# Optimization experiments

Hardware: AMD Instinct MI355X
Metric: run time of the kernel (lower is better)

Reference implementation:

```python
import jax, jax.numpy as jnp
import numpy as np

ROUNDS = 2
N_NODES = 50000
N_EDGES = 800000
NODE_DIM = 128
EDGE_DIM = 32
ACT_DIM = 128


def setup_inputs() -> dict:
    key = jax.random.key(0)
    ks = jax.random.split(key, 10)
    hv = jax.random.normal(ks[0], (N_NODES, NODE_DIM), dtype=jnp.float32)
    he = jax.random.normal(ks[1], (N_EDGES, EDGE_DIM), dtype=jnp.float32)
    src = jax.random.randint(ks[2], (N_EDGES,), 0, N_NODES, dtype=jnp.int32)
    dst = jax.random.randint(ks[3], (N_EDGES,), 0, N_NODES, dtype=jnp.int32)
    cat_dim = 2 * NODE_DIM + EDGE_DIM  # 288
    W_msg = jax.random.normal(ks[4], (ROUNDS, cat_dim, ACT_DIM), dtype=jnp.float32) * 0.05
    b_msg = jax.random.normal(ks[5], (ROUNDS, ACT_DIM), dtype=jnp.float32) * 0.05
    W_ih = jax.random.normal(ks[6], (ROUNDS, ACT_DIM, 3 * NODE_DIM), dtype=jnp.float32) * 0.05
    W_hh = jax.random.normal(ks[7], (ROUNDS, NODE_DIM, 3 * NODE_DIM), dtype=jnp.float32) * 0.05
    b_ih = jax.random.normal(ks[8], (ROUNDS, 3 * NODE_DIM), dtype=jnp.float32) * 0.05
    b_hh = jax.random.normal(ks[9], (ROUNDS, 3 * NODE_DIM), dtype=jnp.float32) * 0.05
    return {"hv": hv, "he": he, "src": src, "dst": dst,
            "W_msg": W_msg, "b_msg": b_msg,
            "W_ih": W_ih, "W_hh": W_hh, "b_ih": b_ih, "b_hh": b_hh}


def _gru_cell(x, h, W_ih, W_hh, b_ih, b_hh):
    # torch.nn.GRUCell math, gate order (r, z, n)
    gi = x @ W_ih + b_ih  # [N, 3H]
    gh = h @ W_hh + b_hh  # [N, 3H]
    ir, iz, in_ = jnp.split(gi, 3, axis=-1)
    hr, hz, hn = jnp.split(gh, 3, axis=-1)
    r = jax.nn.sigmoid(ir + hr)
    z = jax.nn.sigmoid(iz + hz)
    n = jnp.tanh(in_ + r * hn)
    return (1.0 - z) * n + z * h


def reference(hv, he, src, dst, W_msg, b_msg, W_ih, W_hh, b_ih, b_hh):
    N, nd = hv.shape
    for t in range(ROUNDS):
        # Linear on concat([hv_src, hv_dst, he]) == sum of block matmuls
        Ws = W_msg[t, :nd]          # src block
        Wd = W_msg[t, nd:2 * nd]    # dst block
        We = W_msg[t, 2 * nd:]      # edge block
        msg = hv[src] @ Ws + hv[dst] @ Wd + he @ We + b_msg[t]  # [E, act]
        a = jax.ops.segment_sum(msg, dst, num_segments=N)        # per-node sum over incoming edges
        hv = _gru_cell(a, hv, W_ih[t], W_hh[t], b_ih[t], b_hh[t])
    return hv
```

## Files before the change

kernel.cpp:

```cpp
#include <hip/hip_runtime.h>

#define N_NODES 50000
#define N_EDGES 800000
#define ND 128
#define ED 32
#define AD 128
#define CAT 288
#define G3 384

#define XP2 168
#define SCAN_BS 512

typedef unsigned short ushort_t;
typedef __attribute__((ext_vector_type(8))) short bfrag;
typedef __attribute__((ext_vector_type(4))) float f32x4;

__device__ __forceinline__ unsigned int f2bf(float f) {
    unsigned int u = __float_as_uint(f);
    return (u + 0x7FFFu + ((u >> 16) & 1u)) >> 16;
}
__device__ __forceinline__ void split2(float a, float b,
                                       unsigned int& hi, unsigned int& lo) {
    const unsigned int ha = f2bf(a), hb = f2bf(b);
    const float ra = a - __uint_as_float(ha << 16);
    const float rb = b - __uint_as_float(hb << 16);
    hi = ha | (hb << 16);
    lo = f2bf(ra) | (f2bf(rb) << 16);
}
__device__ __forceinline__ void split1(float a, ushort_t& hi, ushort_t& lo) {
    const unsigned int ha = f2bf(a);
    const float ra = a - __uint_as_float(ha << 16);
    hi = (ushort_t)ha;
    lo = (ushort_t)f2bf(ra);
}

__global__ __launch_bounds__(256) void hist_kernel(
    const int* __restrict__ dst, int* __restrict__ deg)
{
    const int e = blockIdx.x * 256 + threadIdx.x;
    if (e < N_EDGES) atomicAdd(&deg[dst[e]], 1);
}

__global__ __launch_bounds__(SCAN_BS) void scan_block_kernel(
    const int* __restrict__ in, int* __restrict__ out,
    int* __restrict__ bsum, int n)
{
    __shared__ int s[SCAN_BS];
    const int g = blockIdx.x * SCAN_BS + threadIdx.x;
    const int v = (g < n) ? in[g] : 0;
    s[threadIdx.x] = v;
    __syncthreads();
    for (int off = 1; off < SCAN_BS; off <<= 1) {
        const int x = (threadIdx.x >= off) ? s[threadIdx.x - off] : 0;
        __syncthreads();
        s[threadIdx.x] += x;
        __syncthreads();
    }
    if (g < n) out[g] = s[threadIdx.x] - v;
    if (threadIdx.x == SCAN_BS - 1) bsum[blockIdx.x] = s[threadIdx.x];
}

__global__ __launch_bounds__(128) void scan_sums_kernel(int* __restrict__ bsum, int nb)
{
    __shared__ int s[128];
    const int i = threadIdx.x;
    s[i] = (i < nb) ? bsum[i] : 0;
    __syncthreads();
    if (i == 0) {
        int acc = 0;
        for (int k = 0; k < nb; ++k) { const int t = s[k]; s[k] = acc; acc += t; }
    }
    __syncthreads();
    if (i < nb) bsum[i] = s[i];
}

__global__ __launch_bounds__(SCAN_BS) void scan_add_kernel(
    int* __restrict__ rowptr, int* __restrict__ cursor,
    const int* __restrict__ bsum, int n)
{
    const int g = blockIdx.x * SCAN_BS + threadIdx.x;
    if (g < n) {
        const int v = rowptr[g] + bsum[blockIdx.x];
        rowptr[g] = v;
        cursor[g] = v;
    }
}

__global__ __launch_bounds__(256) void fill_kernel(
    const int* __restrict__ dst, const int* __restrict__ src,
    int* __restrict__ cursor, int* __restrict__ perm,
    int* __restrict__ src_sorted)
{
    const int e = blockIdx.x * 256 + threadIdx.x;
    if (e < N_EDGES) {
        const int p = atomicAdd(&cursor[dst[e]], 1);
        perm[p] = e;
        src_sorted[p] = src[e];
    }
}

__global__ __launch_bounds__(256) void esum_kernel(
    const float* __restrict__ he, const int* __restrict__ perm,
    const int* __restrict__ rowptr, float* __restrict__ E)
{
    const int id = blockIdx.x * 256 + threadIdx.x;
    if (id >= N_NODES * ED) return;
    const int v = id >> 5, c = id & 31;
    const int r0 = rowptr[v], r1 = rowptr[v + 1];
    float s = 0.f;
    int i = r0;
    for (; i + 4 <= r1; i += 4) {
        const int p0 = perm[i],     p1 = perm[i + 1];
        const int p2 = perm[i + 2], p3 = perm[i + 3];
        const float a = he[(size_t)p0 * ED + c];
        const float b = he[(size_t)p1 * ED + c];
        const float d = he[(size_t)p2 * ED + c];
        const float f = he[(size_t)p3 * ED + c];
        s += (a + b) + (d + f);
    }
    for (; i < r1; ++i)
        s += he[(size_t)perm[i] * ED + c];
    E[(size_t)v * ED + c] = s;
}

__global__ __launch_bounds__(256) void convert_w_kernel(
    const float* __restrict__ W,
    ushort_t* __restrict__ Wt_hi, ushort_t* __restrict__ Wt_lo)
{
    const int id = blockIdx.x * 256 + threadIdx.x;
    if (id >= 2 * CAT * AD) return;
    const int tt = id / (CAT * AD);
    const int q  = id % (CAT * AD);
    const int j  = q & 7;
    const int lr = (q >> 3) & 15;
    const int kq = (q >> 7) & 3;
    const int ks = (q >> 9) % 9;
    const int gnt = q / 4608;
    const int n  = gnt * 16 + lr;
    const int kn = ks * 32 + kq * 8 + j;
    const int ko = kn < 128 ? kn : (kn < 160 ? kn + 128 : kn - 32);
    const float w = W[(size_t)tt * CAT * AD + (size_t)ko * AD + n];
    const unsigned int hi = f2bf(w);
    const float r = w - __uint_as_float(hi << 16);
    const size_t o = (size_t)tt * (CAT * AD) + q;
    Wt_hi[o] = (ushort_t)hi;
    Wt_lo[o] = (ushort_t)f2bf(r);
}

__global__ __launch_bounds__(256) void convert_gatew_kernel(
    const float* __restrict__ W_ih, const float* __restrict__ W_hh,
    ushort_t* __restrict__ Bih_hi, ushort_t* __restrict__ Bih_lo,
    ushort_t* __restrict__ Bhh_hi, ushort_t* __restrict__ Bhh_lo)
{
    const int id = blockIdx.x * 256 + threadIdx.x;
    if (id >= 196608) return;
    const int t   = id / 98304;
    const int rem = id % 98304;
    const int mat = rem / 49152;
    const int q   = rem % 49152;
    const int nt = q / 2048,  r1 = q % 2048;
    const int ks = r1 / 512,  r2 = r1 % 512;
    const int kq = r2 / 128,  r3 = r2 % 128;
    const int lr = r3 / 8,    j  = r3 % 8;
    const int wv = nt / 6, within = nt % 6;
    const int gate = within % 3, hf = within / 3;
    const int n = gate * 128 + wv * 32 + hf * 16 + lr;
    const int k = ks * 32 + kq * 8 + j;
    const float* W = mat ? W_hh : W_ih;
    const float w = W[(size_t)t * ND * G3 + (size_t)k * G3 + n];
    const unsigned int hi = f2bf(w);
    const float res = w - __uint_as_float(hi << 16);
    const size_t o = (size_t)t * 49152 + q;
    if (mat) { Bhh_hi[o] = (ushort_t)hi; Bhh_lo[o] = (ushort_t)f2bf(res); }
    else     { Bih_hi[o] = (ushort_t)hi; Bih_lo[o] = (ushort_t)f2bf(res); }
}

__global__ __launch_bounds__(256) void agg_kernel(
    const float* __restrict__ hv, const int* __restrict__ src_sorted,
    const int* __restrict__ rowptr,
    ushort_t* __restrict__ S_hi, ushort_t* __restrict__ S_lo)
{
    const int v = blockIdx.x * 4 + (threadIdx.x >> 6);
    if (v >= N_NODES) return;
    const int lane = threadIdx.x & 63;
    const int r0 = rowptr[v], r1 = rowptr[v + 1];
    const float2* hv2 = (const float2*)hv;
    float sx = 0.f, sy = 0.f;
    int i = r0;
    for (; i + 8 <= r1; i += 8) {
        const int s0 = src_sorted[i],     s1 = src_sorted[i + 1];
        const int s2 = src_sorted[i + 2], s3 = src_sorted[i + 3];
        const int s4 = src_sorted[i + 4], s5 = src_sorted[i + 5];
        const int s6 = src_sorted[i + 6], s7 = src_sorted[i + 7];
        const float2 a = hv2[(size_t)s0 * 64 + lane];
        const float2 b = hv2[(size_t)s1 * 64 + lane];
        const float2 c = hv2[(size_t)s2 * 64 + lane];
        const float2 d = hv2[(size_t)s3 * 64 + lane];
        const float2 e = hv2[(size_t)s4 * 64 + lane];
        const float2 f = hv2[(size_t)s5 * 64 + lane];
        const float2 g = hv2[(size_t)s6 * 64 + lane];
        const float2 h = hv2[(size_t)s7 * 64 + lane];
        sx += ((a.x + b.x) + (c.x + d.x)) + ((e.x + f.x) + (g.x + h.x));
        sy += ((a.y + b.y) + (c.y + d.y)) + ((e.y + f.y) + (g.y + h.y));
    }
    for (; i < r1; ++i) {
        const float2 a = hv2[(size_t)src_sorted[i] * 64 + lane];
        sx += a.x; sy += a.y;
    }
    unsigned int h, l;
    split2(sx, sy, h, l);
    ((unsigned int*)S_hi)[(size_t)v * 64 + lane] = h;
    ((unsigned int*)S_lo)[(size_t)v * 64 + lane] = l;
}

__global__ __launch_bounds__(256, 3) void fused_msg_gru_kernel(
    const ushort_t* __restrict__ S_hi, const ushort_t* __restrict__ S_lo,
    const float* __restrict__ h_cur, const float* __restrict__ E,
    const int* __restrict__ rowptr,
    const ushort_t* __restrict__ Wt_hi, const ushort_t* __restrict__ Wt_lo,
    const float* __restrict__ bmsg,
    const ushort_t* __restrict__ Bih_hi, const ushort_t* __restrict__ Bih_lo,
    const ushort_t* __restrict__ Bhh_hi, const ushort_t* __restrict__ Bhh_lo,
    const float* __restrict__ b_ih, const float* __restrict__ b_hh,
    float* __restrict__ h_out)
{
    __shared__ __align__(16) char smem[37888];
    ushort_t* xh    = (ushort_t*)smem;
    ushort_t* xl    = xh + 32 * XP2;
    ushort_t* sh_hi = xl + 32 * XP2;
    ushort_t* sh_lo = sh_hi + 32 * 128;
    ushort_t* sa_hi = (ushort_t*)smem;
    ushort_t* sa_lo = sa_hi + 32 * 128;
    __shared__ float sdeg[32];

    const int t    = threadIdx.x;
    const int wave = t >> 6;
    const int lane = t & 63;
    const int kq   = lane >> 4;
    const int lr   = lane & 15;
    const int n0   = blockIdx.x * 32;

    const float mbias0 = bmsg[wave * 32 + lr];
    const float mbias1 = bmsg[wave * 32 + 16 + lr];

    {
        const int row = t >> 3, c8 = t & 7;
        const int n = min(n0 + row, N_NODES - 1);
        if (t < 32) {
            const int nn = min(n0 + t, N_NODES - 1);
            sdeg[t] = (float)(rowptr[nn + 1] - rowptr[nn]);
        }
        {
            const uint4* ph = (const uint4*)(S_hi + (size_t)n * ND + c8 * 16);
            const uint4* pl = (const uint4*)(S_lo + (size_t)n * ND + c8 * 16);
            *(uint4*)&xh[row * XP2 + c8 * 16]     = ph[0];
            *(uint4*)&xh[row * XP2 + c8 * 16 + 8] = ph[1];
            *(uint4*)&xl[row * XP2 + c8 * 16]     = pl[0];
            *(uint4*)&xl[row * XP2 + c8 * 16 + 8] = pl[1];
        }
        {
            const float4* hp = (const float4*)(h_cur + (size_t)n * ND + c8 * 16);
            const float4 v0 = hp[0], v1 = hp[1], v2 = hp[2], v3 = hp[3];
            uint4 h0, h1, l0, l1;
            split2(v0.x, v0.y, h0.x, l0.x); split2(v0.z, v0.w, h0.y, l0.y);
            split2(v1.x, v1.y, h0.z, l0.z); split2(v1.z, v1.w, h0.w, l0.w);
            split2(v2.x, v2.y, h1.x, l1.x); split2(v2.z, v2.w, h1.y, l1.y);
            split2(v3.x, v3.y, h1.z, l1.z); split2(v3.z, v3.w, h1.w, l1.w);
            const int so  = (row * 128 + c8 * 16)     ^ ((row & 7) << 3);
            const int so2 = (row * 128 + c8 * 16 + 8) ^ ((row & 7) << 3);
            *(uint4*)(sh_hi + so)  = h0;  *(uint4*)(sh_hi + so2) = h1;
            *(uint4*)(sh_lo + so)  = l0;  *(uint4*)(sh_lo + so2) = l1;
        }
        {
            const float4 e4 = *(const float4*)(E + (size_t)n * ED + c8 * 4);
            uint2 h0, l0;
            split2(e4.x, e4.y, h0.x, l0.x); split2(e4.z, e4.w, h0.y, l0.y);
            *(uint2*)&xh[row * XP2 + 128 + c8 * 4] = h0;
            *(uint2*)&xl[row * XP2 + 128 + c8 * 4] = l0;
        }
    }
    __syncthreads();

    f32x4 aX00 = {0.f,0.f,0.f,0.f}, aX01 = {0.f,0.f,0.f,0.f};
    f32x4 aX10 = {0.f,0.f,0.f,0.f}, aX11 = {0.f,0.f,0.f,0.f};
    f32x4 aP00 = {0.f,0.f,0.f,0.f}, aP01 = {0.f,0.f,0.f,0.f};
    f32x4 aP10 = {0.f,0.f,0.f,0.f}, aP11 = {0.f,0.f,0.f,0.f};
    {
        const size_t wb0 = (size_t)(wave * 2 + 0) * 4608 + kq * 128 + lr * 8;
        const size_t wb1 = (size_t)(wave * 2 + 1) * 4608 + kq * 128 + lr * 8;
        const ushort_t* wh0 = Wt_hi + wb0;  const ushort_t* wl0 = Wt_lo + wb0;
        const ushort_t* wh1 = Wt_hi + wb1;  const ushort_t* wl1 = Wt_lo + wb1;
        #pragma unroll
        for (int ks = 0; ks < 5; ++ks) {
            const int ko = ks * 32 + kq * 8;
            const bfrag a0h = *(const bfrag*)&xh[lr * XP2 + ko];
            const bfrag a0l = *(const bfrag*)&xl[lr * XP2 + ko];
            const bfrag a1h = *(const bfrag*)&xh[(16 + lr) * XP2 + ko];
            const bfrag a1l = *(const bfrag*)&xl[(16 + lr) * XP2 + ko];
            const bfrag b0h = *(const bfrag*)(wh0 + ks * 512);
            const bfrag b0l = *(const bfrag*)(wl0 + ks * 512);
            const bfrag b1h = *(const bfrag*)(wh1 + ks * 512);
            const bfrag b1l = *(const bfrag*)(wl1 + ks * 512);
            aX00 = __builtin_amdgcn_mfma_f32_16x16x32_bf16(a0h, b0h, aX00, 0, 0, 0);
            aX00 = __builtin_amdgcn_mfma_f32_16x16x32_bf16(a0l, b0h, aX00, 0, 0, 0);
            aX00 = __builtin_amdgcn_mfma_f32_16x16x32_bf16(a0h, b0l, aX00, 0, 0, 0);
            aX01 = __builtin_amdgcn_mfma_f32_16x16x32_bf16(a0h, b1h, aX01, 0, 0, 0);
            aX01 = __builtin_amdgcn_mfma_f32_16x16x32_bf16(a0l, b1h, aX01, 0, 0, 0);
            aX01 = __builtin_amdgcn_mfma_f32_16x16x32_bf16(a0h, b1l, aX01, 0, 0, 0);
            aX10 = __builtin_amdgcn_mfma_f32_16x16x32_bf16(a1h, b0h, aX10, 0, 0, 0);
            aX10 = __builtin_amdgcn_mfma_f32_16x16x32_bf16(a1l, b0h, aX10, 0, 0, 0);
            aX10 = __builtin_amdgcn_mfma_f32_16x16x32_bf16(a1h, b0l, aX10, 0, 0, 0);
            aX11 = __builtin_amdgcn_mfma_f32_16x16x32_bf16(a1h, b1h, aX11, 0, 0, 0);
            aX11 = __builtin_amdgcn_mfma_f32_16x16x32_bf16(a1l, b1h, aX11, 0, 0, 0);
            aX11 = __builtin_amdgcn_mfma_f32_16x16x32_bf16(a1h, b1l, aX11, 0, 0, 0);
        }
        #pragma unroll
        for (int ks = 5; ks < 9; ++ks) {
            const int hk = (ks - 5) * 32 + kq * 8;
            const int o0 = (lr * 128 + hk)        ^ ((lr & 7) << 3);
            const int o1 = ((16 + lr) * 128 + hk) ^ ((lr & 7) << 3);
            const bfrag a0h = *(const bfrag*)(sh_hi + o0);
            const bfrag a0l = *(const bfrag*)(sh_lo + o0);
            const bfrag a1h = *(const bfrag*)(sh_hi + o1);
            const bfrag a1l = *(const bfrag*)(sh_lo + o1);
            const bfrag b0h = *(const bfrag*)(wh0 + ks * 512);
            const bfrag b0l = *(const bfrag*)(wl0 + ks * 512);
            const bfrag b1h = *(const bfrag*)(wh1 + ks * 512);
            const bfrag b1l = *(const bfrag*)(wl1 + ks * 512);
            aP00 = __builtin_amdgcn_mfma_f32_16x16x32_bf16(a0h, b0h, aP00, 0, 0, 0);
            aP00 = __builtin_amdgcn_mfma_f32_16x16x32_bf16(a0l, b0h, aP00, 0, 0, 0);
            aP00 = __builtin_amdgcn_mfma_f32_16x16x32_bf16(a0h, b0l, aP00, 0, 0, 0);
            aP01 = __builtin_amdgcn_mfma_f32_16x16x32_bf16(a0h, b1h, aP01, 0, 0, 0);
            aP01 = __builtin_amdgcn_mfma_f32_16x16x32_bf16(a0l, b1h, aP01, 0, 0, 0);
            aP01 = __builtin_amdgcn_mfma_f32_16x16x32_bf16(a0h, b1l, aP01, 0, 0, 0);
            aP10 = __builtin_amdgcn_mfma_f32_16x16x32_bf16(a1h, b0h, aP10, 0, 0, 0);
            aP10 = __builtin_amdgcn_mfma_f32_16x16x32_bf16(a1l, b0h, aP10, 0, 0, 0);
            aP10 = __builtin_amdgcn_mfma_f32_16x16x32_bf16(a1h, b0l, aP10, 0, 0, 0);
            aP11 = __builtin_amdgcn_mfma_f32_16x16x32_bf16(a1h, b1h, aP11, 0, 0, 0);
            aP11 = __builtin_amdgcn_mfma_f32_16x16x32_bf16(a1l, b1h, aP11, 0, 0, 0);
            aP11 = __builtin_amdgcn_mfma_f32_16x16x32_bf16(a1h, b1l, aP11, 0, 0, 0);
        }
    }
    __syncthreads();

    #pragma unroll
    for (int r = 0; r < 4; ++r) {
        const int row0 = kq * 4 + r;
        const int row1 = 16 + row0;
        const int c0 = wave * 32 + lr, c1 = c0 + 16;
        const float d0 = sdeg[row0], d1 = sdeg[row1];
        ushort_t h, l;
        split1(aX00[r] + d0 * (aP00[r] + mbias0), h, l);
        { const int o = (row0 * 128 + c0) ^ ((row0 & 7) << 3); sa_hi[o] = h; sa_lo[o] = l; }
        split1(aX01[r] + d0 * (aP01[r] + mbias1), h, l);
        { const int o = (row0 * 128 + c1) ^ ((row0 & 7) << 3); sa_hi[o] = h; sa_lo[o] = l; }
        split1(aX10[r] + d1 * (aP10[r] + mbias0), h, l);
        { const int o = (row1 * 128 + c0) ^ ((row1 & 7) << 3); sa_hi[o] = h; sa_lo[o] = l; }
        split1(aX11[r] + d1 * (aP11[r] + mbias1), h, l);
        { const int o = (row1 * 128 + c1) ^ ((row1 & 7) << 3); sa_hi[o] = h; sa_lo[o] = l; }
    }
    __syncthreads();

    #pragma unroll
    for (int half = 0; half < 2; ++half) {
        f32x4 ai[2][3], ah2[2][3];
        #pragma unroll
        for (int m = 0; m < 2; ++m)
            #pragma unroll
            for (int g = 0; g < 3; ++g) {
                ai[m][g]  = (f32x4){0.f, 0.f, 0.f, 0.f};
                ah2[m][g] = (f32x4){0.f, 0.f, 0.f, 0.f};
            }
        #pragma unroll
        for (int ks = 0; ks < 4; ++ks) {
            bfrag afh[2], afl[2], hfh[2], hfl[2];
            #pragma unroll
            for (int m = 0; m < 2; ++m) {
                const int o = ((m * 16 + lr) * 128 + ks * 32 + kq * 8) ^ ((lr & 7) << 3);
                afh[m] = *(const bfrag*)(sa_hi + o);
                afl[m] = *(const bfrag*)(sa_lo + o);
                hfh[m] = *(const bfrag*)(sh_hi + o);
                hfl[m] = *(const bfrag*)(sh_lo + o);
            }
            #pragma unroll
            for (int g = 0; g < 3; ++g) {
                const int gnt = wave * 6 + half * 3 + g;
                const size_t bo = (size_t)(gnt * 2048 + ks * 512 + kq * 128 + lr * 8);
                const bfrag bih_h = *(const bfrag*)(Bih_hi + bo);
                const bfrag bih_l = *(const bfrag*)(Bih_lo + bo);
                const bfrag bhh_h = *(const bfrag*)(Bhh_hi + bo);
                const bfrag bhh_l = *(const bfrag*)(Bhh_lo + bo);
                #pragma unroll
                for (int m = 0; m < 2; ++m) {
                    ai[m][g]  = __builtin_amdgcn_mfma_f32_16x16x32_bf16(afh[m], bih_h, ai[m][g], 0, 0, 0);
                    ai[m][g]  = __builtin_amdgcn_mfma_f32_16x16x32_bf16(afl[m], bih_h, ai[m][g], 0, 0, 0);
                    ai[m][g]  = __builtin_amdgcn_mfma_f32_16x16x32_bf16(afh[m], bih_l, ai[m][g], 0, 0, 0);
                    ah2[m][g] = __builtin_amdgcn_mfma_f32_16x16x32_bf16(hfh[m], bhh_h, ah2[m][g], 0, 0, 0);
                    ah2[m][g] = __builtin_amdgcn_mfma_f32_16x16x32_bf16(hfl[m], bhh_h, ah2[m][g], 0, 0, 0);
                    ah2[m][g] = __builtin_amdgcn_mfma_f32_16x16x32_bf16(hfh[m], bhh_l, ah2[m][g], 0, 0, 0);
                }
            }
        }
        const int c = wave * 32 + half * 16 + lr;
        const float br  = b_ih[c] + b_hh[c];
        const float bz  = b_ih[128 + c] + b_hh[128 + c];
        const float bin = b_ih[256 + c];
        const float bhn = b_hh[256 + c];
        #pragma unroll
        for (int m = 0; m < 2; ++m)
            #pragma unroll
            for (int r = 0; r < 4; ++r) {
                const int nn = n0 + m * 16 + kq * 4 + r;
                if (nn < N_NODES) {
                    const float hc = h_cur[(size_t)nn * ND + c];
                    const float rg = 1.f / (1.f + __expf(-(ai[m][0][r] + ah2[m][0][r] + br)));
                    const float zg = 1.f / (1.f + __expf(-(ai[m][1][r] + ah2[m][1][r] + bz)));
                    const float npre = ai[m][2][r] + bin + rg * (ah2[m][2][r] + bhn);
                    const float ng = 1.f - 2.f / (__expf(2.f * npre) + 1.f);
                    h_out[(size_t)nn * ND + c] = (1.f - zg) * ng + zg * hc;
                }
            }
    }
}

extern "C" void kernel_launch(void* const* d_in, const int* in_sizes, int n_in,
                              void* d_out, int out_size, void* d_ws, size_t ws_size,
                              hipStream_t stream)
{
    const float* hv   = (const float*)d_in[0];
    const float* he   = (const float*)d_in[1];
    const int*   src  = (const int*)d_in[2];
    const int*   dst  = (const int*)d_in[3];
    const float* Wmsg = (const float*)d_in[4];
    const float* bmsg = (const float*)d_in[5];
    const float* Wih  = (const float*)d_in[6];
    const float* Whh  = (const float*)d_in[7];
    const float* bih  = (const float*)d_in[8];
    const float* bhh  = (const float*)d_in[9];
    float* out = (float*)d_out;

    const int nscan = ((N_NODES + SCAN_BS - 1) / SCAN_BS) * SCAN_BS;
    const int nblk  = nscan / SCAN_BS;

    char* p = (char*)d_ws;
    ushort_t* S_hi = (ushort_t*)p;            p += (size_t)N_NODES * ND * 2;
    ushort_t* S_lo = (ushort_t*)p;            p += (size_t)N_NODES * ND * 2;
    float* E = (float*)p;                     p += (size_t)N_NODES * ED * 4;
    ushort_t* Wt_hi = (ushort_t*)p;           p += (size_t)2 * AD * CAT * 2;
    ushort_t* Wt_lo = (ushort_t*)p;           p += (size_t)2 * AD * CAT * 2;
    ushort_t* Bih_hi = (ushort_t*)p;          p += (size_t)2 * G3 * ND * 2;
    ushort_t* Bih_lo = (ushort_t*)p;          p += (size_t)2 * G3 * ND * 2;
    ushort_t* Bhh_hi = (ushort_t*)p;          p += (size_t)2 * G3 * ND * 2;
    ushort_t* Bhh_lo = (ushort_t*)p;          p += (size_t)2 * G3 * ND * 2;
    int* deg    = (int*)p;                    p += (size_t)nscan * 4;
    int* rowptr = (int*)p;                    p += (size_t)nscan * 4;
    int* cursor = (int*)p;                    p += (size_t)nscan * 4;
    int* bsum   = (int*)p;                    p += 128 * 4;
    int* perm   = (int*)p;                    p += (size_t)N_EDGES * 4;
    int* src_sorted = (int*)p;                p += (size_t)N_EDGES * 4;

    convert_w_kernel<<<(2 * CAT * AD + 255) / 256, 256, 0, stream>>>(Wmsg, Wt_hi, Wt_lo);
    convert_gatew_kernel<<<768, 256, 0, stream>>>(Wih, Whh, Bih_hi, Bih_lo, Bhh_hi, Bhh_lo);

    hipMemsetAsync(deg, 0, (size_t)nscan * 4, stream);
    hist_kernel<<<(N_EDGES + 255) / 256, 256, 0, stream>>>(dst, deg);
    scan_block_kernel<<<nblk, SCAN_BS, 0, stream>>>(deg, rowptr, bsum, nscan);
    scan_sums_kernel<<<1, 128, 0, stream>>>(bsum, nblk);
    scan_add_kernel<<<nblk, SCAN_BS, 0, stream>>>(rowptr, cursor, bsum, nscan);
    fill_kernel<<<(N_EDGES + 255) / 256, 256, 0, stream>>>(dst, src, cursor, perm, src_sorted);
    esum_kernel<<<(N_NODES * ED + 255) / 256, 256, 0, stream>>>(he, perm, rowptr, E);

    const int tile_blocks = (N_NODES + 31) / 32;

    for (int t = 0; t < 2; ++t) {
        const float* h_cur = (t == 0) ? hv : out;
        agg_kernel<<<(N_NODES + 3) / 4, 256, 0, stream>>>(
            h_cur, src_sorted, rowptr, S_hi, S_lo);
        fused_msg_gru_kernel<<<tile_blocks, 256, 0, stream>>>(
            S_hi, S_lo, h_cur, E, rowptr,
            Wt_hi + (size_t)t * AD * CAT, Wt_lo + (size_t)t * AD * CAT,
            bmsg + (size_t)t * AD,
            Bih_hi + (size_t)t * G3 * ND, Bih_lo + (size_t)t * G3 * ND,
            Bhh_hi + (size_t)t * G3 * ND, Bhh_lo + (size_t)t * G3 * ND,
            bih + (size_t)t * G3, bhh + (size_t)t * G3, out);
    }
}
```

Baseline: 528.8 us.

## Enlarge fused GRU tile to 64 nodes and stage output through shared memory

Doubles the node tile per block from 32 to 64 rows, so each weight fragment loaded from global memory feeds four MFMA row tiles instead of two. The r/z gate input and hidden products are folded into one accumulator, which cuts register use. Outputs are staged in shared memory and written back as coalesced float4 rows. The cost is twice the LDS per block, launch bounds lowered from 3 to 2 blocks per CU, and extra syncs, so latency hiding may drop.

```diff
diff --git a/kernel.cpp b/kernel.cpp
--- a/kernel.cpp
+++ b/kernel.cpp
@@ -8,6 +8,7 @@
 #define CAT 288
 #define G3 384
 
+#define MT 64
 #define XP2 168
 #define SCAN_BS 512
 
@@ -213,7 +214,7 @@
     ((unsigned int*)S_lo)[(size_t)v * 64 + lane] = l;
 }
 
-__global__ __launch_bounds__(256, 3) void fused_msg_gru_kernel(
+__global__ __launch_bounds__(256, 2) void fused_msg_gru_kernel(
     const ushort_t* __restrict__ S_hi, const ushort_t* __restrict__ S_lo,
     const float* __restrict__ h_cur, const float* __restrict__ E,
     const int* __restrict__ rowptr,
@@ -224,67 +225,75 @@
     const float* __restrict__ b_ih, const float* __restrict__ b_hh,
     float* __restrict__ h_out)
 {
-    __shared__ __align__(16) char smem[37888];
+    __shared__ __align__(16) char smem[75776];
     ushort_t* xh    = (ushort_t*)smem;
-    ushort_t* xl    = xh + 32 * XP2;
-    ushort_t* sh_hi = xl + 32 * XP2;
-    ushort_t* sh_lo = sh_hi + 32 * 128;
+    ushort_t* xl    = xh + MT * XP2;
+    ushort_t* sh_hi = xl + MT * XP2;
+    ushort_t* sh_lo = sh_hi + MT * 128;
     ushort_t* sa_hi = (ushort_t*)smem;
-    ushort_t* sa_lo = sa_hi + 32 * 128;
-    __shared__ float sdeg[32];
+    ushort_t* sa_lo = sa_hi + MT * 128;
+    float* out_s = (float*)smem;
+    __shared__ float sdeg[MT];
 
     const int t    = threadIdx.x;
     const int wave = t >> 6;
     const int lane = t & 63;
     const int kq   = lane >> 4;
     const int lr   = lane & 15;
-    const int n0   = blockIdx.x * 32;
+    const int n0   = blockIdx.x * MT;
 
     const float mbias0 = bmsg[wave * 32 + lr];
     const float mbias1 = bmsg[wave * 32 + 16 + lr];
 
     {
-        const int row = t >> 3, c8 = t & 7;
+        const int row = t >> 2, q = t & 3;
         const int n = min(n0 + row, N_NODES - 1);
-        if (t < 32) {
+        if (t < MT) {
             const int nn = min(n0 + t, N_NODES - 1);
             sdeg[t] = (float)(rowptr[nn + 1] - rowptr[nn]);
         }
         {
-            const uint4* ph = (const uint4*)(S_hi + (size_t)n * ND + c8 * 16);
-            const uint4* pl = (const uint4*)(S_lo + (size_t)n * ND + c8 * 16);
-            *(uint4*)&xh[row * XP2 + c8 * 16]     = ph[0];
-            *(uint4*)&xh[row * XP2 + c8 * 16 + 8] = ph[1];
-            *(uint4*)&xl[row * XP2 + c8 * 16]     = pl[0];
-            *(uint4*)&xl[row * XP2 + c8 * 16 + 8] = pl[1];
+            const uint4* ph = (const uint4*)(S_hi + (size_t)n * ND + q * 32);
+            const uint4* pl = (const uint4*)(S_lo + (size_t)n * ND + q * 32);
+            #pragma unroll
+            for (int j = 0; j < 4; ++j) {
+                *(uint4*)&xh[row * XP2 + q * 32 + j * 8] = ph[j];
+                *(uint4*)&xl[row * XP2 + q * 32 + j * 8] = pl[j];
+            }
         }
         {
-            const float4* hp = (const float4*)(h_cur + (size_t)n * ND + c8 * 16);
-            const float4 v0 = hp[0], v1 = hp[1], v2 = hp[2], v3 = hp[3];
-            uint4 h0, h1, l0, l1;
-            split2(v0.x, v0.y, h0.x, l0.x); split2(v0.z, v0.w, h0.y, l0.y);
-            split2(v1.x, v1.y, h0.z, l0.z); split2(v1.z, v1.w, h0.w, l0.w);
-            split2(v2.x, v2.y, h1.x, l1.x); split2(v2.z, v2.w, h1.y, l1.y);
-            split2(v3.x, v3.y, h1.z, l1.z); split2(v3.z, v3.w, h1.w, l1.w);
-            const int so  = (row * 128 + c8 * 16)     ^ ((row & 7) << 3);
-            const int so2 = (row * 128 + c8 * 16 + 8) ^ ((row & 7) << 3);
-            *(uint4*)(sh_hi + so)  = h0;  *(uint4*)(sh_hi + so2) = h1;
-            *(uint4*)(sh_lo + so)  = l0;  *(uint4*)(sh_lo + so2) = l1;
+            const float4* hp = (const float4*)(h_cur + (size_t)n * ND + q * 32);
+            #pragma unroll
+            for (int j = 0; j < 4; ++j) {
+                const float4 va = hp[2 * j], vb = hp[2 * j + 1];
+                uint4 hh, ll;
+                split2(va.x, va.y, hh.x, ll.x); split2(va.z, va.w, hh.y, ll.y);
+                split2(vb.x, vb.y, hh.z, ll.z); split2(vb.z, vb.w, hh.w, ll.w);
+                const int so = (row * 128 + q * 32 + j * 8) ^ ((row & 7) << 3);
+                *(uint4*)(sh_hi + so) = hh;
+                *(uint4*)(sh_lo + so) = ll;
+            }
         }
         {
-            const float4 e4 = *(const float4*)(E + (size_t)n * ED + c8 * 4);
-            uint2 h0, l0;
-            split2(e4.x, e4.y, h0.x, l0.x); split2(e4.z, e4.w, h0.y, l0.y);
-            *(uint2*)&xh[row * XP2 + 128 + c8 * 4] = h0;
-            *(uint2*)&xl[row * XP2 + 128 + c8 * 4] = l0;
-        }
-    }
-    __syncthreads();
-
-    f32x4 aX00 = {0.f,0.f,0.f,0.f}, aX01 = {0.f,0.f,0.f,0.f};
-    f32x4 aX10 = {0.f,0.f,0.f,0.f}, aX11 = {0.f,0.f,0.f,0.f};
-    f32x4 aP00 = {0.f,0.f,0.f,0.f}, aP01 = {0.f,0.f,0.f,0.f};
-    f32x4 aP10 = {0.f,0.f,0.f,0.f}, aP11 = {0.f,0.f,0.f,0.f};
+            const float4 e0 = *(const float4*)(E + (size_t)n * ED + q * 8);
+            const float4 e1 = *(const float4*)(E + (size_t)n * ED + q * 8 + 4);
+            uint4 eh, el;
+            split2(e0.x, e0.y, eh.x, el.x); split2(e0.z, e0.w, eh.y, el.y);
+            split2(e1.x, e1.y, eh.z, el.z); split2(e1.z, e1.w, eh.w, el.w);
+            *(uint4*)&xh[row * XP2 + 128 + q * 8] = eh;
+            *(uint4*)&xl[row * XP2 + 128 + q * 8] = el;
+        }
+    }
+    __syncthreads();
+
+    f32x4 aX[4][2], aP[4][2];
+    #pragma unroll
+    for (int m = 0; m < 4; ++m)
+        #pragma unroll
+        for (int nt = 0; nt < 2; ++nt) {
+            aX[m][nt] = (f32x4){0.f, 0.f, 0.f, 0.f};
+            aP[m][nt] = (f32x4){0.f, 0.f, 0.f, 0.f};
+        }
     {
         const size_t wb0 = (size_t)(wave * 2 + 0) * 4608 + kq * 128 + lr * 8;
         const size_t wb1 = (size_t)(wave * 2 + 1) * 4608 + kq * 128 + lr * 8;
@@ -293,89 +302,76 @@
         #pragma unroll
         for (int ks = 0; ks < 5; ++ks) {
             const int ko = ks * 32 + kq * 8;
-            const bfrag a0h = *(const bfrag*)&xh[lr * XP2 + ko];
-            const bfrag a0l = *(const bfrag*)&xl[lr * XP2 + ko];
-            const bfrag a1h = *(const bfrag*)&xh[(16 + lr) * XP2 + ko];
-            const bfrag a1l = *(const bfrag*)&xl[(16 + lr) * XP2 + ko];
             const bfrag b0h = *(const bfrag*)(wh0 + ks * 512);
             const bfrag b0l = *(const bfrag*)(wl0 + ks * 512);
             const bfrag b1h = *(const bfrag*)(wh1 + ks * 512);
             const bfrag b1l = *(const bfrag*)(wl1 + ks * 512);
-            aX00 = __builtin_amdgcn_mfma_f32_16x16x32_bf16(a0h, b0h, aX00, 0, 0, 0);
-            aX00 = __builtin_amdgcn_mfma_f32_16x16x32_bf16(a0l, b0h, aX00, 0, 0, 0);
-            aX00 = __builtin_amdgcn_mfma_f32_16x16x32_bf16(a0h, b0l, aX00, 0, 0, 0);
-            aX01 = __builtin_amdgcn_mfma_f32_16x16x32_bf16(a0h, b1h, aX01, 0, 0, 0);
-            aX01 = __builtin_amdgcn_mfma_f32_16x16x32_bf16(a0l, b1h, aX01, 0, 0, 0);
-            aX01 = __builtin_amdgcn_mfma_f32_16x16x32_bf16(a0h, b1l, aX01, 0, 0, 0);
-            aX10 = __builtin_amdgcn_mfma_f32_16x16x32_bf16(a1h, b0h, aX10, 0, 0, 0);
-            aX10 = __builtin_amdgcn_mfma_f32_16x16x32_bf16(a1l, b0h, aX10, 0, 0, 0);
-            aX10 = __builtin_amdgcn_mfma_f32_16x16x32_bf16(a1h, b0l, aX10, 0, 0, 0);
-            aX11 = __builtin_amdgcn_mfma_f32_16x16x32_bf16(a1h, b1h, aX11, 0, 0, 0);
-            aX11 = __builtin_amdgcn_mfma_f32_16x16x32_bf16(a1l, b1h, aX11, 0, 0, 0);
-            aX11 = __builtin_amdgcn_mfma_f32_16x16x32_bf16(a1h, b1l, aX11, 0, 0, 0);
+            #pragma unroll
+            for (int m = 0; m < 4; ++m) {
+                const bfrag ah_ = *(const bfrag*)&xh[(m * 16 + lr) * XP2 + ko];
+                const bfrag al_ = *(const bfrag*)&xl[(m * 16 + lr) * XP2 + ko];
+                aX[m][0] = __builtin_amdgcn_mfma_f32_16x16x32_bf16(ah_, b0h, aX[m][0], 0, 0, 0);
+                aX[m][0] = __builtin_amdgcn_mfma_f32_16x16x32_bf16(al_, b0h, aX[m][0], 0, 0, 0);
+                aX[m][0] = __builtin_amdgcn_mfma_f32_16x16x32_bf16(ah_, b0l, aX[m][0], 0, 0, 0);
+                aX[m][1] = __builtin_amdgcn_mfma_f32_16x16x32_bf16(ah_, b1h, aX[m][1], 0, 0, 0);
+                aX[m][1] = __builtin_amdgcn_mfma_f32_16x16x32_bf16(al_, b1h, aX[m][1], 0, 0, 0);
+                aX[m][1] = __builtin_amdgcn_mfma_f32_16x16x32_bf16(ah_, b1l, aX[m][1], 0, 0, 0);
+            }
         }
         #pragma unroll
         for (int ks = 5; ks < 9; ++ks) {
             const int hk = (ks - 5) * 32 + kq * 8;
-            const int o0 = (lr * 128 + hk)        ^ ((lr & 7) << 3);
-            const int o1 = ((16 + lr) * 128 + hk) ^ ((lr & 7) << 3);
-            const bfrag a0h = *(const bfrag*)(sh_hi + o0);
-            const bfrag a0l = *(const bfrag*)(sh_lo + o0);
-            const bfrag a1h = *(const bfrag*)(sh_hi + o1);
-            const bfrag a1l = *(const bfrag*)(sh_lo + o1);
             const bfrag b0h = *(const bfrag*)(wh0 + ks * 512);
             const bfrag b0l = *(const bfrag*)(wl0 + ks * 512);
             const bfrag b1h = *(const bfrag*)(wh1 + ks * 512);
             const bfrag b1l = *(const bfrag*)(wl1 + ks * 512);
-            aP00 = __builtin_amdgcn_mfma_f32_16x16x32_bf16(a0h, b0h, aP00, 0, 0, 0);
-            aP00 = __builtin_amdgcn_mfma_f32_16x16x32_bf16(a0l, b0h, aP00, 0, 0, 0);
-            aP00 = __builtin_amdgcn_mfma_f32_16x16x32_bf16(a0h, b0l, aP00, 0, 0, 0);
-            aP01 = __builtin_amdgcn_mfma_f32_16x16x32_bf16(a0h, b1h, aP01, 0, 0, 0);
-            aP01 = __builtin_amdgcn_mfma_f32_16x16x32_bf16(a0l, b1h, aP01, 0, 0, 0);
-            aP01 = __builtin_amdgcn_mfma_f32_16x16x32_bf16(a0h, b1l, aP01, 0, 0, 0);
-            aP10 = __builtin_amdgcn_mfma_f32_16x16x32_bf16(a1h, b0h, aP10, 0, 0, 0);
-            aP10 = __builtin_amdgcn_mfma_f32_16x16x32_bf16(a1l, b0h, aP10, 0, 0, 0);
-            aP10 = __builtin_amdgcn_mfma_f32_16x16x32_bf16(a1h, b0l, aP10, 0, 0, 0);
-            aP11 = __builtin_amdgcn_mfma_f32_16x16x32_bf16(a1h, b1h, aP11, 0, 0, 0);
-            aP11 = __builtin_amdgcn_mfma_f32_16x16x32_bf16(a1l, b1h, aP11, 0, 0, 0);
-            aP11 = __builtin_amdgcn_mfma_f32_16x16x32_bf16(a1h, b1l, aP11, 0, 0, 0);
+            #pragma unroll
+            for (int m = 0; m < 4; ++m) {
+                const int o = ((m * 16 + lr) * 128 + hk) ^ ((lr & 7) << 3);
+                const bfrag ah_ = *(const bfrag*)(sh_hi + o);
+                const bfrag al_ = *(const bfrag*)(sh_lo + o);
+                aP[m][0] = __builtin_amdgcn_mfma_f32_16x16x32_bf16(ah_, b0h, aP[m][0], 0, 0, 0);
+                aP[m][0] = __builtin_amdgcn_mfma_f32_16x16x32_bf16(al_, b0h, aP[m][0], 0, 0, 0);
+                aP[m][0] = __builtin_amdgcn_mfma_f32_16x16x32_bf16(ah_, b0l, aP[m][0], 0, 0, 0);
+                aP[m][1] = __builtin_amdgcn_mfma_f32_16x16x32_bf16(ah_, b1h, aP[m][1], 0, 0, 0);
+                aP[m][1] = __builtin_amdgcn_mfma_f32_16x16x32_bf16(al_, b1h, aP[m][1], 0, 0, 0);
+                aP[m][1] = __builtin_amdgcn_mfma_f32_16x16x32_bf16(ah_, b1l, aP[m][1], 0, 0, 0);
+            }
         }
     }
     __syncthreads();
 
     #pragma unroll
-    for (int r = 0; r < 4; ++r) {
-        const int row0 = kq * 4 + r;
-        const int row1 = 16 + row0;
-        const int c0 = wave * 32 + lr, c1 = c0 + 16;
-        const float d0 = sdeg[row0], d1 = sdeg[row1];
-        ushort_t h, l;
-        split1(aX00[r] + d0 * (aP00[r] + mbias0), h, l);
-        { const int o = (row0 * 128 + c0) ^ ((row0 & 7) << 3); sa_hi[o] = h; sa_lo[o] = l; }
-        split1(aX01[r] + d0 * (aP01[r] + mbias1), h, l);
-        { const int o = (row0 * 128 + c1) ^ ((row0 & 7) << 3); sa_hi[o] = h; sa_lo[o] = l; }
-        split1(aX10[r] + d1 * (aP10[r] + mbias0), h, l);
-        { const int o = (row1 * 128 + c0) ^ ((row1 & 7) << 3); sa_hi[o] = h; sa_lo[o] = l; }
-        split1(aX11[r] + d1 * (aP11[r] + mbias1), h, l);
-        { const int o = (row1 * 128 + c1) ^ ((row1 & 7) << 3); sa_hi[o] = h; sa_lo[o] = l; }
-    }
-    __syncthreads();
-
+    for (int m = 0; m < 4; ++m)
+        #pragma unroll
+        for (int r = 0; r < 4; ++r) {
+            const int row = m * 16 + kq * 4 + r;
+            const int c0 = wave * 32 + lr, c1 = c0 + 16;
+            const float d = sdeg[row];
+            ushort_t h, l;
+            split1(aX[m][0][r] + d * (aP[m][0][r] + mbias0), h, l);
+            { const int o = (row * 128 + c0) ^ ((row & 7) << 3); sa_hi[o] = h; sa_lo[o] = l; }
+            split1(aX[m][1][r] + d * (aP[m][1][r] + mbias1), h, l);
+            { const int o = (row * 128 + c1) ^ ((row & 7) << 3); sa_hi[o] = h; sa_lo[o] = l; }
+        }
+    __syncthreads();
+
+    float outv[2][4][4];
     #pragma unroll
     for (int half = 0; half < 2; ++half) {
-        f32x4 ai[2][3], ah2[2][3];
-        #pragma unroll
-        for (int m = 0; m < 2; ++m)
-            #pragma unroll
-            for (int g = 0; g < 3; ++g) {
-                ai[m][g]  = (f32x4){0.f, 0.f, 0.f, 0.f};
-                ah2[m][g] = (f32x4){0.f, 0.f, 0.f, 0.f};
-            }
+        f32x4 arz[4][2], anI[4], anH[4];
+        #pragma unroll
+        for (int m = 0; m < 4; ++m) {
+            arz[m][0] = (f32x4){0.f, 0.f, 0.f, 0.f};
+            arz[m][1] = (f32x4){0.f, 0.f, 0.f, 0.f};
+            anI[m]    = (f32x4){0.f, 0.f, 0.f, 0.f};
+            anH[m]    = (f32x4){0.f, 0.f, 0.f, 0.f};
+        }
         #pragma unroll
         for (int ks = 0; ks < 4; ++ks) {
-            bfrag afh[2], afl[2], hfh[2], hfl[2];
-            #pragma unroll
-            for (int m = 0; m < 2; ++m) {
+            bfrag afh[4], afl[4], hfh[4], hfl[4];
+            #pragma unroll
+            for (int m = 0; m < 4; ++m) {
                 const int o = ((m * 16 + lr) * 128 + ks * 32 + kq * 8) ^ ((lr & 7) << 3);
                 afh[m] = *(const bfrag*)(sa_hi + o);
                 afl[m] = *(const bfrag*)(sa_lo + o);
@@ -390,14 +386,28 @@
                 const bfrag bih_l = *(const bfrag*)(Bih_lo + bo);
                 const bfrag bhh_h = *(const bfrag*)(Bhh_hi + bo);
                 const bfrag bhh_l = *(const bfrag*)(Bhh_lo + bo);
-                #pragma unroll
-                for (int m = 0; m < 2; ++m) {
-                    ai[m][g]  = __builtin_amdgcn_mfma_f32_16x16x32_bf16(afh[m], bih_h, ai[m][g], 0, 0, 0);
-                    ai[m][g]  = __builtin_amdgcn_mfma_f32_16x16x32_bf16(afl[m], bih_h, ai[m][g], 0, 0, 0);
-                    ai[m][g]  = __builtin_amdgcn_mfma_f32_16x16x32_bf16(afh[m], bih_l, ai[m][g], 0, 0, 0);
-                    ah2[m][g] = __builtin_amdgcn_mfma_f32_16x16x32_bf16(hfh[m], bhh_h, ah2[m][g], 0, 0, 0);
-                    ah2[m][g] = __builtin_amdgcn_mfma_f32_16x16x32_bf16(hfl[m], bhh_h, ah2[m][g], 0, 0, 0);
-                    ah2[m][g] = __builtin_amdgcn_mfma_f32_16x16x32_bf16(hfh[m], bhh_l, ah2[m][g], 0, 0, 0);
+                if (g < 2) {
+                    #pragma unroll
+                    for (int m = 0; m < 4; ++m) {
+                        f32x4 a = arz[m][g];
+                        a = __builtin_amdgcn_mfma_f32_16x16x32_bf16(afh[m], bih_h, a, 0, 0, 0);
+                        a = __builtin_amdgcn_mfma_f32_16x16x32_bf16(afl[m], bih_h, a, 0, 0, 0);
+                        a = __builtin_amdgcn_mfma_f32_16x16x32_bf16(afh[m], bih_l, a, 0, 0, 0);
+                        a = __builtin_amdgcn_mfma_f32_16x16x32_bf16(hfh[m], bhh_h, a, 0, 0, 0);
+                        a = __builtin_amdgcn_mfma_f32_16x16x32_bf16(hfl[m], bhh_h, a, 0, 0, 0);
+                        a = __builtin_amdgcn_mfma_f32_16x16x32_bf16(hfh[m], bhh_l, a, 0, 0, 0);
+                        arz[m][g] = a;
+                    }
+                } else {
+                    #pragma unroll
+                    for (int m = 0; m < 4; ++m) {
+                        anI[m] = __builtin_amdgcn_mfma_f32_16x16x32_bf16(afh[m], bih_h, anI[m], 0, 0, 0);
+                        anI[m] = __builtin_amdgcn_mfma_f32_16x16x32_bf16(afl[m], bih_h, anI[m], 0, 0, 0);
+                        anI[m] = __builtin_amdgcn_mfma_f32_16x16x32_bf16(afh[m], bih_l, anI[m], 0, 0, 0);
+                        anH[m] = __builtin_amdgcn_mfma_f32_16x16x32_bf16(hfh[m], bhh_h, anH[m], 0, 0, 0);
+                        anH[m] = __builtin_amdgcn_mfma_f32_16x16x32_bf16(hfl[m], bhh_h, anH[m], 0, 0, 0);
+                        anH[m] = __builtin_amdgcn_mfma_f32_16x16x32_bf16(hfh[m], bhh_l, anH[m], 0, 0, 0);
+                    }
                 }
             }
         }
@@ -407,19 +417,39 @@
         const float bin = b_ih[256 + c];
         const float bhn = b_hh[256 + c];
         #pragma unroll
-        for (int m = 0; m < 2; ++m)
+        for (int m = 0; m < 4; ++m)
             #pragma unroll
             for (int r = 0; r < 4; ++r) {
-                const int nn = n0 + m * 16 + kq * 4 + r;
-                if (nn < N_NODES) {
-                    const float hc = h_cur[(size_t)nn * ND + c];
-                    const float rg = 1.f / (1.f + __expf(-(ai[m][0][r] + ah2[m][0][r] + br)));
-                    const float zg = 1.f / (1.f + __expf(-(ai[m][1][r] + ah2[m][1][r] + bz)));
-                    const float npre = ai[m][2][r] + bin + rg * (ah2[m][2][r] + bhn);
-                    const float ng = 1.f - 2.f / (__expf(2.f * npre) + 1.f);
-                    h_out[(size_t)nn * ND + c] = (1.f - zg) * ng + zg * hc;
-                }
-            }
+                const int nn = min(n0 + m * 16 + kq * 4 + r, N_NODES - 1);
+                const float hc = h_cur[(size_t)nn * ND + c];
+                const float rg = 1.f / (1.f + __expf(-(arz[m][0][r] + br)));
+                const float zg = 1.f / (1.f + __expf(-(arz[m][1][r] + bz)));
+                const float npre = anI[m][r] + bin + rg * (anH[m][r] + bhn);
+                const float ng = 1.f - 2.f / (__expf(2.f * npre) + 1.f);
+                outv[half][m][r] = (1.f - zg) * ng + zg * hc;
+            }
+    }
+    __syncthreads();
+
+    #pragma unroll
+    for (int half = 0; half < 2; ++half) {
+        const int c = wave * 32 + half * 16 + lr;
+        #pragma unroll
+        for (int m = 0; m < 4; ++m)
+            #pragma unroll
+            for (int r = 0; r < 4; ++r)
+                out_s[(m * 16 + kq * 4 + r) * 132 + c] = outv[half][m][r];
+    }
+    __syncthreads();
+    #pragma unroll
+    for (int i = 0; i < 8; ++i) {
+        const int idx = i * 256 + t;
+        const int rw = idx >> 5, c4 = (idx & 31) * 4;
+        const int nn = n0 + rw;
+        if (nn < N_NODES) {
+            const float4 v = *(const float4*)&out_s[rw * 132 + c4];
+            *(float4*)&h_out[(size_t)nn * ND + c4] = v;
+        }
     }
 }
 
@@ -470,7 +500,7 @@
     fill_kernel<<<(N_EDGES + 255) / 256, 256, 0, stream>>>(dst, src, cursor, perm, src_sorted);
     esum_kernel<<<(N_NODES * ED + 255) / 256, 256, 0, stream>>>(he, perm, rowptr, E);
 
-    const int tile_blocks = (N_NODES + 31) / 32;
+    const int tile_blocks = (N_NODES + MT - 1) / MT;
 
     for (int t = 0; t < 2; ++t) {
         const float* h_cur = (t == 0) ? hv : out;
```

Measured after the change: 625.9 us. +18.4%, slower.
